# Kernel tuning notes

Hardware: AMD Instinct MI355X
Metric: run time of the kernel (lower is better)

Reference implementation:

```python
import jax, jax.numpy as jnp
import numpy as np

N_HEAD = 16  # matches init_kwargs
LN_EPS = 1e-5


def setup_inputs() -> dict:
    key = jax.random.key(0)
    k0, k1, k2 = jax.random.split(key, 3)
    S, B, D = 2048, 2, 1024
    N, Dh = N_HEAD, D // N_HEAD
    h = jax.random.normal(k0, (S, B, D), dtype=jnp.float32)
    # causal mask, True = masked; source's dim==3 branch: shape [qlen, klen, batch]
    causal = jnp.triu(jnp.ones((S, S), dtype=bool), k=1)
    attn_mask = jnp.broadcast_to(causal[:, :, None], (S, S, B))
    W_qkv = jax.random.normal(k1, (D, 3 * N * Dh), dtype=jnp.float32) * (1.0 / np.sqrt(D))
    W_o = jax.random.normal(k2, (N * Dh, D), dtype=jnp.float32) * (1.0 / np.sqrt(N * Dh))
    gamma = jnp.ones((D,), dtype=jnp.float32)
    beta = jnp.zeros((D,), dtype=jnp.float32)
    return {"h": h, "attn_mask": attn_mask, "W_qkv": W_qkv, "W_o": W_o,
            "gamma": gamma, "beta": beta}


def reference(h, attn_mask, W_qkv, W_o, gamma, beta):
    # h: [S, B, D] (seq, batch, d_model) -- Transformer-XL layout
    S, B, D = h.shape
    N = N_HEAD
    Dh = W_o.shape[0] // N
    scale = 1.0 / np.sqrt(Dh)

    qkv = h @ W_qkv                                   # [S, B, 3*N*Dh]
    q, k, v = jnp.split(qkv, 3, axis=-1)
    q = q.reshape(S, B, N, Dh)
    k = k.reshape(S, B, N, Dh)
    v = v.reshape(S, B, N, Dh)

    # attention scores: [i, j, b, n]
    score = jnp.einsum('ibnd,jbnd->ijbn', q, k) * scale
    # mask (dim==3 branch of source): attn_mask [i, j, b] -> [i, j, b, 1]
    score = jnp.where(attn_mask[:, :, :, None], -jnp.inf, score)
    prob = jax.nn.softmax(score, axis=1)              # softmax over key axis j

    attn_vec = jnp.einsum('ijbn,jbnd->ibnd', prob, v).reshape(S, B, N * Dh)
    attn_out = attn_vec @ W_o                         # [S, B, D]

    # residual + LayerNorm (biased variance, like torch.nn.LayerNorm)
    x = h + attn_out
    mu = jnp.mean(x, axis=-1, keepdims=True)
    var = jnp.mean(jnp.square(x - mu), axis=-1, keepdims=True)
    out = (x - mu) * jax.lax.rsqrt(var + LN_EPS) * gamma + beta
    return out
```

## Files before the change

kernel.cpp:

```cpp
#include <hip/hip_runtime.h>

typedef unsigned short u16;
typedef unsigned int u32;
typedef __attribute__((ext_vector_type(8))) __bf16 bf16x8;
typedef __attribute__((ext_vector_type(4))) float f32x4;
typedef __attribute__((ext_vector_type(8))) unsigned short u16x8;
typedef __attribute__((ext_vector_type(4))) unsigned short u16x4;
typedef __attribute__((ext_vector_type(2))) unsigned int u32x2;
typedef __attribute__((ext_vector_type(4))) unsigned int u32x4;

#if defined(__has_builtin)
#if __has_builtin(__builtin_amdgcn_permlane32_swap) && __has_builtin(__builtin_amdgcn_permlane16_swap)
#define USE_PERMLANE 1
#endif
#endif
#ifndef USE_PERMLANE
#define USE_PERMLANE 0
#endif

__device__ __forceinline__ u16 f2bf(float f) {
    u32 u = __builtin_bit_cast(u32, f);
    u += 0x7fffu + ((u >> 16) & 1u);
    return (u16)(u >> 16);
}

__device__ __forceinline__ float fexp2(float x) {
#if __has_builtin(__builtin_amdgcn_exp2f)
    return __builtin_amdgcn_exp2f(x);
#else
    return exp2f(x);
#endif
}

__device__ __forceinline__ float frcp(float x) {
#if __has_builtin(__builtin_amdgcn_rcpf)
    return __builtin_amdgcn_rcpf(x);
#else
    return 1.0f / x;
#endif
}

__global__ __launch_bounds__(256) void conv_h_kernel(const float* __restrict__ h,
                                                     u16* __restrict__ hb) {
    int i = blockIdx.x * 256 + threadIdx.x;
    float4 v = ((const float4*)h)[i];
    u16x4 o = { f2bf(v.x), f2bf(v.y), f2bf(v.z), f2bf(v.w) };
    ((u16x4*)hb)[i] = o;
}

__global__ __launch_bounds__(256) void conv_wt_kernel(const float* __restrict__ W,
                                                      u16* __restrict__ Wt,
                                                      int R, int C,
                                                      int scale_rows, float scale) {
    __shared__ float tile[32][33];
    int t = threadIdx.x;
    int r = t >> 3, c4 = (t & 7) * 4;
    int gx = blockIdx.x * 32, gy = blockIdx.y * 32;
    float4 v = *(const float4*)&W[(size_t)(gy + r) * C + gx + c4];
    tile[r][c4 + 0] = v.x; tile[r][c4 + 1] = v.y;
    tile[r][c4 + 2] = v.z; tile[r][c4 + 3] = v.w;
    __syncthreads();
    float sc = (gx + r < scale_rows) ? scale : 1.0f;
    u16x4 o = { f2bf(tile[c4 + 0][r] * sc), f2bf(tile[c4 + 1][r] * sc),
                f2bf(tile[c4 + 2][r] * sc), f2bf(tile[c4 + 3][r] * sc) };
    *(u16x4*)&Wt[(size_t)(gx + r) * R + gy + c4] = o;
}

template <int MODE>
__global__ __launch_bounds__(256) void gemm_bt_kernel(
        const u16* __restrict__ A, const u16* __restrict__ Bt,
        u16* __restrict__ Cb, const float* __restrict__ H, float* __restrict__ X,
        int M, int N, int K) {
    constexpr int LDT = 40;
    __shared__ u16 alds[2][128 * LDT];
    __shared__ u16 blds[2][128 * LDT];
    const int t = threadIdx.x;
    const int lane = t & 63;
    const int wave = t >> 6;
    const int wm = wave >> 1, wn = wave & 1;
    const int m0 = blockIdx.x * 128;
    const int n0 = blockIdx.y * 128;
    const int nk = K >> 5;

    const int srow = t >> 1;
    const int sch = (t & 1) * 2;
    const u16* ga = A + (size_t)(m0 + srow) * K + sch * 8;
    const u16* gb = Bt + (size_t)(n0 + srow) * K + sch * 8;
    const int wo = srow * LDT + sch * 8;

    u16x8 ra0 = *(const u16x8*)(ga);
    u16x8 ra1 = *(const u16x8*)(ga + 8);
    u16x8 rb0 = *(const u16x8*)(gb);
    u16x8 rb1 = *(const u16x8*)(gb + 8);
    *(u16x8*)&alds[0][wo] = ra0;  *(u16x8*)&alds[0][wo + 8] = ra1;
    *(u16x8*)&blds[0][wo] = rb0;  *(u16x8*)&blds[0][wo + 8] = rb1;

    f32x4 acc[4][4] = {};
    const int ko = (lane >> 4) * 8;
    const int arow_base = wm * 64 + (lane & 15);
    const int brow_base = wn * 64 + (lane & 15);

    int cur = 0;
    for (int kt = 0; kt < nk; ++kt) {
        __syncthreads();
        if (kt + 1 < nk) {
            const u16* gan = ga + (kt + 1) * 32;
            const u16* gbn = gb + (kt + 1) * 32;
            ra0 = *(const u16x8*)(gan);
            ra1 = *(const u16x8*)(gan + 8);
            rb0 = *(const u16x8*)(gbn);
            rb1 = *(const u16x8*)(gbn + 8);
        }
        bf16x8 afrag[4], bfrag[4];
#pragma unroll
        for (int m = 0; m < 4; ++m)
            afrag[m] = *(const bf16x8*)&alds[cur][(arow_base + m * 16) * LDT + ko];
#pragma unroll
        for (int n = 0; n < 4; ++n)
            bfrag[n] = *(const bf16x8*)&blds[cur][(brow_base + n * 16) * LDT + ko];
#pragma unroll
        for (int m = 0; m < 4; ++m)
#pragma unroll
            for (int n = 0; n < 4; ++n)
                acc[m][n] = __builtin_amdgcn_mfma_f32_16x16x32_bf16(afrag[m], bfrag[n],
                                                                   acc[m][n], 0, 0, 0);
        if (kt + 1 < nk) {
            *(u16x8*)&alds[cur ^ 1][wo] = ra0;  *(u16x8*)&alds[cur ^ 1][wo + 8] = ra1;
            *(u16x8*)&blds[cur ^ 1][wo] = rb0;  *(u16x8*)&blds[cur ^ 1][wo + 8] = rb1;
        }
        cur ^= 1;
    }

#pragma unroll
    for (int m = 0; m < 4; ++m)
#pragma unroll
        for (int n = 0; n < 4; ++n)
#pragma unroll
            for (int r = 0; r < 4; ++r) {
                int row = m0 + wm * 64 + m * 16 + (lane >> 4) * 4 + r;
                int col = n0 + wn * 64 + n * 16 + (lane & 15);
                size_t idx = (size_t)row * N + col;
                if (MODE == 0) Cb[idx] = f2bf(acc[m][n][r]);
                else           X[idx] = acc[m][n][r] + H[idx];
            }
}

__global__ __launch_bounds__(256) void transpose_v_kernel(const u16* __restrict__ qkvb,
                                                          u16* __restrict__ vt) {
    __shared__ u16 tl[64][72];
    const int t = threadIdx.x;
    const int p = blockIdx.y;
    const int nn = p >> 1, b = p & 1;
    const int s0 = blockIdx.x * 64;
    const int r = t >> 2;
    const int ch = (t & 3) * 2;
    const u16* g = qkvb + ((size_t)(s0 + r) * 2 + b) * 3072 + 2048 + nn * 64;
    *(u16x8*)&tl[r][ch * 8]     = *(const u16x8*)(g + ch * 8);
    *(u16x8*)&tl[r][ch * 8 + 8] = *(const u16x8*)(g + ch * 8 + 8);
    __syncthreads();
    const int dh = t >> 2;
    const int sc = (t & 3) * 2;
    u16* o = vt + ((size_t)p * 64 + dh) * 2048 + s0;
#pragma unroll
    for (int q = 0; q < 2; ++q) {
        int scq = sc + q;
        u16x8 v;
#pragma unroll
        for (int j = 0; j < 8; ++j) v[j] = tl[scq * 8 + j][dh];
        *(u16x8*)(o + scq * 8) = v;
    }
}

__global__ __launch_bounds__(256) void attn_kernel(const u16* __restrict__ qkvb,
                                                   const u16* __restrict__ vt,
                                                   u16* __restrict__ attnb) {
    constexpr int LKT = 72;
    __shared__ u16 klds[2][64 * LKT];
    __shared__ u16 vlds[2][64 * LKT];
#if !USE_PERMLANE
    __shared__ u16 plds[4][16 * LKT];
#endif
    const int t = threadIdx.x;
    const int lane = t & 63;
    const int w = t >> 6;
    const int bid = blockIdx.x;
    const int g = bid >> 5;
    const int sq = g & 7, jq = g >> 3;
    const int qt = (jq == 0) ? (31 - sq) : (jq == 1) ? (16 + sq)
                 : (jq == 2) ? (15 - sq) : sq;
    const int p = bid & 31;
    const int nn = p >> 1, b = p & 1;
    const int i0 = qt * 64;

    const int li = lane & 15;
    const int lg = lane >> 4;

    const int qrow = i0 + w * 16 + li;
    const u16* qg = qkvb + ((size_t)qrow * 2 + b) * 3072 + nn * 64 + lg * 8;
    bf16x8 qa0 = *(const bf16x8*)(qg);
    bf16x8 qa1 = *(const bf16x8*)(qg + 32);

    f32x4 o[4] = {};
    float mrun = -3.0e38f;
    float lrun = 0.f;

    const int srow = t >> 2;
    const int sch = (t & 3) * 2;
    const u16* kg = qkvb + 1024 + nn * 64 + sch * 8;
    const u16* vg = vt + ((size_t)p * 64 + srow) * 2048 + sch * 8;
    const int swo = srow * LKT + sch * 8;

    const int nt = qt + 1;
    u16x8 k0, k1, v0, v1;
    {
        const u16* kgp = kg + ((size_t)srow * 2 + b) * 3072;
        k0 = *(const u16x8*)(kgp);  k1 = *(const u16x8*)(kgp + 8);
        v0 = *(const u16x8*)(vg);   v1 = *(const u16x8*)(vg + 8);
    }
    *(u16x8*)&klds[0][swo] = k0;  *(u16x8*)&klds[0][swo + 8] = k1;
    *(u16x8*)&vlds[0][swo] = v0;  *(u16x8*)&vlds[0][swo + 8] = v1;
    __syncthreads();

    for (int jt = 0; jt < nt; ++jt) {
        const int buf = jt & 1;
        if (jt + 1 < nt) {
            const u16* kgp = kg + ((size_t)(jt * 64 + 64 + srow) * 2 + b) * 3072;
            k0 = *(const u16x8*)(kgp);  k1 = *(const u16x8*)(kgp + 8);
            const u16* vgp = vg + jt * 64 + 64;
            v0 = *(const u16x8*)(vgp);  v1 = *(const u16x8*)(vgp + 8);
        }

        f32x4 st[4];
        __builtin_amdgcn_s_setprio(1);
#pragma unroll
        for (int cf = 0; cf < 4; ++cf) {
            bf16x8 kb0 = *(const bf16x8*)&klds[buf][(cf * 16 + li) * LKT + lg * 8];
            bf16x8 kb1 = *(const bf16x8*)&klds[buf][(cf * 16 + li) * LKT + 32 + lg * 8];
            f32x4 z = {};
            z = __builtin_amdgcn_mfma_f32_16x16x32_bf16(kb0, qa0, z, 0, 0, 0);
            z = __builtin_amdgcn_mfma_f32_16x16x32_bf16(kb1, qa1, z, 0, 0, 0);
            st[cf] = z;
        }
        __builtin_amdgcn_s_setprio(0);

        if (jt == qt) {
            const int it = w * 16 + li;
#pragma unroll
            for (int cf = 0; cf < 4; ++cf)
#pragma unroll
                for (int r = 0; r < 4; ++r) {
                    int jl = cf * 16 + lg * 4 + r;
                    if (jl > it) st[cf][r] = -3.0e38f;
                }
        }

        float mloc = st[0][0];
#pragma unroll
        for (int cf = 0; cf < 4; ++cf)
#pragma unroll
            for (int r = 0; r < 4; ++r) mloc = fmaxf(mloc, st[cf][r]);
        mloc = fmaxf(mloc, __shfl_xor(mloc, 16, 64));
        mloc = fmaxf(mloc, __shfl_xor(mloc, 32, 64));

        if (__any(mloc > mrun + 8.0f)) {
            float mnew = fmaxf(mrun, mloc);
            float alpha = fexp2(mrun - mnew);
            lrun *= alpha;
            mrun = mnew;
#pragma unroll
            for (int r = 0; r < 4; ++r) {
                float ar = __shfl(alpha, lg * 4 + r, 64);
#pragma unroll
                for (int cf = 0; cf < 4; ++cf) o[cf][r] *= ar;
            }
        }

#if USE_PERMLANE
        float rsum = 0.f;
        u32 wv[4][2];
#pragma unroll
        for (int cf = 0; cf < 4; ++cf)
#pragma unroll
            for (int rr = 0; rr < 2; ++rr) {
                float p0 = fexp2(st[cf][2 * rr] - mrun);
                float p1 = fexp2(st[cf][2 * rr + 1] - mrun);
                rsum += p0 + p1;
                u32 wres;
                asm("v_cvt_pk_bf16_f32 %0, %1, %2" : "=v"(wres) : "v"(p0), "v"(p1));
                wv[cf][rr] = wres;
            }
        rsum += __shfl_xor(rsum, 16, 64);
        rsum += __shfl_xor(rsum, 32, 64);
        lrun += rsum;

        __builtin_amdgcn_s_setprio(1);
#pragma unroll
        for (int ks = 0; ks < 2; ++ks) {
            u32x2 sa = __builtin_amdgcn_permlane32_swap(wv[2 * ks][0], wv[2 * ks + 1][0], false, false);
            u32x2 fa = __builtin_amdgcn_permlane16_swap(sa[0], sa[1], false, false);
            u32x2 sb = __builtin_amdgcn_permlane32_swap(wv[2 * ks][1], wv[2 * ks + 1][1], false, false);
            u32x2 fb = __builtin_amdgcn_permlane16_swap(sb[0], sb[1], false, false);
            u32x4 fw = { fa[0], fb[0], fa[1], fb[1] };
            bf16x8 pa = __builtin_bit_cast(bf16x8, fw);
#pragma unroll
            for (int cf = 0; cf < 4; ++cf) {
                bf16x8 vb = *(const bf16x8*)&vlds[buf][(cf * 16 + li) * LKT + ks * 32 + lg * 8];
                o[cf] = __builtin_amdgcn_mfma_f32_16x16x32_bf16(pa, vb, o[cf], 0, 0, 0);
            }
        }
        __builtin_amdgcn_s_setprio(0);
#else
        float rsum = 0.f;
#pragma unroll
        for (int cf = 0; cf < 4; ++cf) {
            u16x4 pw;
#pragma unroll
            for (int r = 0; r < 4; ++r) {
                float pv = fexp2(st[cf][r] - mrun);
                rsum += pv;
                pw[r] = f2bf(pv);
            }
            *(u16x4*)&plds[w][li * LKT + cf * 16 + lg * 4] = pw;
        }
        rsum += __shfl_xor(rsum, 16, 64);
        rsum += __shfl_xor(rsum, 32, 64);
        lrun += rsum;

        asm volatile("s_waitcnt lgkmcnt(0)" ::: "memory");
        __builtin_amdgcn_sched_barrier(0);

#pragma unroll
        for (int ks = 0; ks < 2; ++ks) {
            bf16x8 pa = *(const bf16x8*)&plds[w][li * LKT + ks * 32 + lg * 8];
#pragma unroll
            for (int cf = 0; cf < 4; ++cf) {
                bf16x8 vb = *(const bf16x8*)&vlds[buf][(cf * 16 + li) * LKT + ks * 32 + lg * 8];
                o[cf] = __builtin_amdgcn_mfma_f32_16x16x32_bf16(pa, vb, o[cf], 0, 0, 0);
            }
        }
#endif

        if (jt + 1 < nt) {
            *(u16x8*)&klds[buf ^ 1][swo] = k0;  *(u16x8*)&klds[buf ^ 1][swo + 8] = k1;
            *(u16x8*)&vlds[buf ^ 1][swo] = v0;  *(u16x8*)&vlds[buf ^ 1][swo + 8] = v1;
        }
        __syncthreads();
    }

    float rinv = frcp(lrun);
#pragma unroll
    for (int r = 0; r < 4; ++r) {
        float rv = __shfl(rinv, lg * 4 + r, 64);
        int srowg = i0 + w * 16 + lg * 4 + r;
        u16* og = attnb + ((size_t)srowg * 2 + b) * 1024 + nn * 64;
#pragma unroll
        for (int cf = 0; cf < 4; ++cf)
            og[cf * 16 + li] = f2bf(o[cf][r] * rv);
    }
}

__global__ __launch_bounds__(256) void ln_kernel(const float* __restrict__ X,
                                                 const float* __restrict__ gamma,
                                                 const float* __restrict__ beta,
                                                 float* __restrict__ out) {
    __shared__ float red[8];
    const int t = threadIdx.x;
    const int row = blockIdx.x;
    float4 v = ((const float4*)(X + (size_t)row * 1024))[t];
    float s = v.x + v.y + v.z + v.w;
#pragma unroll
    for (int off = 1; off < 64; off <<= 1) s += __shfl_xor(s, off, 64);
    if ((t & 63) == 0) red[t >> 6] = s;
    __syncthreads();
    float mu = (red[0] + red[1] + red[2] + red[3]) * (1.f / 1024.f);
    float dx = v.x - mu, dy = v.y - mu, dz = v.z - mu, dw = v.w - mu;
    float q = dx * dx + dy * dy + dz * dz + dw * dw;
#pragma unroll
    for (int off = 1; off < 64; off <<= 1) q += __shfl_xor(q, off, 64);
    if ((t & 63) == 0) red[4 + (t >> 6)] = q;
    __syncthreads();
    float var = (red[4] + red[5] + red[6] + red[7]) * (1.f / 1024.f);
    float rs = rsqrtf(var + 1e-5f);
    float4 g = ((const float4*)gamma)[t];
    float4 bt = ((const float4*)beta)[t];
    float4 o;
    o.x = dx * rs * g.x + bt.x;
    o.y = dy * rs * g.y + bt.y;
    o.z = dz * rs * g.z + bt.z;
    o.w = dw * rs * g.w + bt.w;
    ((float4*)(out + (size_t)row * 1024))[t] = o;
}

extern "C" void kernel_launch(void* const* d_in, const int* in_sizes, int n_in,
                              void* d_out, int out_size, void* d_ws, size_t ws_size,
                              hipStream_t stream) {
    const float* h     = (const float*)d_in[0];
    const float* Wqkv  = (const float*)d_in[2];
    const float* Wo    = (const float*)d_in[3];
    const float* gamma = (const float*)d_in[4];
    const float* beta  = (const float*)d_in[5];
    float* out = (float*)d_out;

    char* ws = (char*)d_ws;
    u16*   hb    = (u16*)(ws);
    u16*   wqkvt = (u16*)(ws + 8388608);
    u16*   wot   = (u16*)(ws + 14680064);
    u16*   qkvb  = (u16*)(ws + 16777216);
    u16*   vt    = (u16*)(ws + 41943040);
    u16*   attnb = (u16*)(ws + 50331648);
    float* xbuf  = (float*)(ws + 58720256);

    const float qscale = 0.125f * 1.44269504088896f;

    conv_h_kernel<<<4096, 256, 0, stream>>>(h, hb);
    conv_wt_kernel<<<dim3(96, 32), 256, 0, stream>>>(Wqkv, wqkvt, 1024, 3072, 1024, qscale);
    conv_wt_kernel<<<dim3(32, 32), 256, 0, stream>>>(Wo, wot, 1024, 1024, 0, 1.0f);
    gemm_bt_kernel<0><<<dim3(32, 24), 256, 0, stream>>>(hb, wqkvt, qkvb, nullptr, nullptr,
                                                        4096, 3072, 1024);
    transpose_v_kernel<<<dim3(32, 32), 256, 0, stream>>>(qkvb, vt);
    attn_kernel<<<1024, 256, 0, stream>>>(qkvb, vt, attnb);
    gemm_bt_kernel<1><<<dim3(32, 8), 256, 0, stream>>>(attnb, wot, nullptr, h, xbuf,
                                                       4096, 1024, 1024);
    ln_kernel<<<4096, 256, 0, stream>>>(xbuf, gamma, beta, out);
}
```

Baseline: 117.7 us.

## Replace QKV GEMM with 256x256 tiled, 8-phase pipelined global_load_lds kernel

```diff
diff --git a/kernel.cpp b/kernel.cpp
--- a/kernel.cpp
+++ b/kernel.cpp
@@ -39,6 +39,10 @@
     return 1.0f / x;
 #endif
 }
+
+#define GL16(gp, lp) __builtin_amdgcn_global_load_lds(                           \
+    (const __attribute__((address_space(1))) void*)(gp),                          \
+    (__attribute__((address_space(3))) void*)(lp), 16, 0, 0)
 
 __global__ __launch_bounds__(256) void conv_h_kernel(const float* __restrict__ h,
                                                      u16* __restrict__ hb) {
@@ -66,6 +70,121 @@
     *(u16x4*)&Wt[(size_t)(gx + r) * R + gy + c4] = o;
 }
 
+__global__ __launch_bounds__(512, 2) void gemm1_8ph_kernel(
+        const u16* __restrict__ A, const u16* __restrict__ Bt,
+        u16* __restrict__ Cb, int M, int N, int K) {
+    __shared__ u16 alds[2][2][8192];
+    __shared__ u16 blds[2][2][8192];
+    const int t = threadIdx.x;
+    const int lane = t & 63;
+    const int wave = t >> 6;
+    const int wm = wave >> 2;
+    const int wn = wave & 3;
+    const int li = lane & 15, lg = lane >> 4;
+
+    const int nwg = (int)gridDim.x;
+    const int lin = (int)blockIdx.x;
+    const int swz = (lin & 7) * (nwg >> 3) + (lin >> 3);
+    const int mt = M >> 8;
+    const int m0 = (swz % mt) << 8;
+    const int n0 = (swz / mt) << 8;
+
+    const int srow = lane >> 2;
+    const int sslot = ((lane & 3) ^ ((lane >> 2) & 3)) * 8;
+    const u16* gAb = A + (size_t)(m0 + wave * 32 + srow) * K + sslot;
+    const u16* gBb = Bt + (size_t)(n0 + wave * 32 + srow) * K + sslot;
+    const int ldst = wave * 1024;
+
+#define STAGE_A1(buf, ks, kt)                                                    \
+    { GL16(gAb + (size_t)(kt) * 64 + (ks) * 32, &alds[buf][ks][ldst]);           \
+      GL16(gAb + (size_t)16 * K + (size_t)(kt) * 64 + (ks) * 32,                 \
+           &alds[buf][ks][ldst + 512]); }
+#define STAGE_B1(buf, ks, kt)                                                    \
+    { GL16(gBb + (size_t)(kt) * 64 + (ks) * 32, &blds[buf][ks][ldst]);           \
+      GL16(gBb + (size_t)16 * K + (size_t)(kt) * 64 + (ks) * 32,                 \
+           &blds[buf][ks][ldst + 512]); }
+
+    const int rslot = (lg ^ (li & 3)) * 8;
+#define READ_A(buf, ks, mh)                                                      \
+    _Pragma("unroll") for (int m = 0; m < 4; ++m)                                \
+        af[m] = *(const bf16x8*)&alds[buf][ks][(wm * 128 + (mh) * 64 + m * 16 + li) * 32 + rslot];
+#define READ_B(buf, ks)                                                          \
+    _Pragma("unroll") for (int n = 0; n < 4; ++n)                                \
+        bfr[n] = *(const bf16x8*)&blds[buf][ks][(wn * 64 + n * 16 + li) * 32 + rslot];
+#define MFMA16(mh)                                                               \
+    _Pragma("unroll") for (int m = 0; m < 4; ++m)                                \
+        _Pragma("unroll") for (int n = 0; n < 4; ++n)                            \
+            acc[(mh) * 4 + m][n] = __builtin_amdgcn_mfma_f32_16x16x32_bf16(      \
+                af[m], bfr[n], acc[(mh) * 4 + m][n], 0, 0, 0);
+
+#define PH_BAR() __builtin_amdgcn_s_barrier()
+#define PH_MFMA(mh)                                                              \
+    PH_BAR();                                                                    \
+    __builtin_amdgcn_s_setprio(1); MFMA16(mh); __builtin_amdgcn_s_setprio(0);    \
+    PH_BAR();
+#define VMCNT4() asm volatile("s_waitcnt vmcnt(4)" ::: "memory")
+
+    f32x4 acc[8][4] = {};
+    bf16x8 af[4], bfr[4];
+
+    STAGE_A1(0, 0, 0); STAGE_B1(0, 0, 0);
+    STAGE_A1(0, 1, 0); STAGE_B1(0, 1, 0);
+    STAGE_A1(1, 0, 1); STAGE_B1(1, 0, 1);
+    VMCNT4();
+    PH_BAR();
+
+    const int NIT = K >> 7;
+    for (int i = 0; i < NIT; ++i) {
+        const int t1 = 2 * i + 1, t2 = 2 * i + 2, t3 = 2 * i + 3;
+        const bool more = (i + 1 < NIT);
+        READ_A(0, 0, 0); READ_B(0, 0);
+        STAGE_A1(1, 1, t1);
+        PH_MFMA(0);
+        READ_A(0, 0, 1);
+        STAGE_B1(1, 1, t1);
+        PH_MFMA(1);
+        READ_A(0, 1, 0); READ_B(0, 1);
+        if (more) STAGE_A1(0, 0, t2);
+        PH_MFMA(0);
+        READ_A(0, 1, 1);
+        if (more) STAGE_B1(0, 0, t2);
+        VMCNT4();
+        PH_MFMA(1);
+        READ_A(1, 0, 0); READ_B(1, 0);
+        if (more) STAGE_A1(0, 1, t2);
+        PH_MFMA(0);
+        READ_A(1, 0, 1);
+        if (more) STAGE_B1(0, 1, t2);
+        PH_MFMA(1);
+        READ_A(1, 1, 0); READ_B(1, 1);
+        if (more) STAGE_A1(1, 0, t3);
+        PH_MFMA(0);
+        READ_A(1, 1, 1);
+        if (more) STAGE_B1(1, 0, t3);
+        VMCNT4();
+        PH_MFMA(1);
+    }
+
+#pragma unroll
+    for (int mr = 0; mr < 8; ++mr)
+#pragma unroll
+        for (int nr = 0; nr < 4; ++nr)
+#pragma unroll
+            for (int rr = 0; rr < 4; ++rr) {
+                int row = m0 + wm * 128 + mr * 16 + lg * 4 + rr;
+                int col = n0 + wn * 64 + nr * 16 + li;
+                Cb[(size_t)row * N + col] = f2bf(acc[mr][nr][rr]);
+            }
+#undef STAGE_A1
+#undef STAGE_B1
+#undef READ_A
+#undef READ_B
+#undef MFMA16
+#undef PH_BAR
+#undef PH_MFMA
+#undef VMCNT4
+}
+
 template <int MODE>
 __global__ __launch_bounds__(256) void gemm_bt_kernel(
         const u16* __restrict__ A, const u16* __restrict__ Bt,
@@ -415,8 +534,7 @@
     conv_h_kernel<<<4096, 256, 0, stream>>>(h, hb);
     conv_wt_kernel<<<dim3(96, 32), 256, 0, stream>>>(Wqkv, wqkvt, 1024, 3072, 1024, qscale);
     conv_wt_kernel<<<dim3(32, 32), 256, 0, stream>>>(Wo, wot, 1024, 1024, 0, 1.0f);
-    gemm_bt_kernel<0><<<dim3(32, 24), 256, 0, stream>>>(hb, wqkvt, qkvb, nullptr, nullptr,
-                                                        4096, 3072, 1024);
+    gemm1_8ph_kernel<<<192, 512, 0, stream>>>(hb, wqkvt, qkvb, 4096, 3072, 1024);
     transpose_v_kernel<<<dim3(32, 32), 256, 0, stream>>>(qkvb, vt);
     attn_kernel<<<1024, 256, 0, stream>>>(qkvb, vt, attnb);
     gemm_bt_kernel<1><<<dim3(32, 8), 256, 0, stream>>>(attnb, wot, nullptr, h, xbuf,
```

Result: slower. 124.7 us (+5.9%).
